# Kernel tuning notes

Hardware: AMD Instinct MI355X
Metric: run time of the kernel (lower is better)

Reference implementation:

```python
import jax, jax.numpy as jnp
import numpy as np

D_HIDDEN = 512
N_HEADS = 8
D_HEAD = D_HIDDEN // N_HEADS
LAYER_IDX = 0
FACTOR = 0.5 / float(np.sqrt(D_HEAD))


def setup_inputs() -> dict:
    key = jax.random.key(0)
    ks = jax.random.split(key, 16)
    B, N, d = 4, 2048, D_HIDDEN
    s = 1.0 / float(np.sqrt(d))
    inp = {
        "H": jax.random.normal(ks[0], (B, N, d), jnp.float32),
        "V": jax.random.normal(ks[1], (B, N, 3, d), jnp.float32),
        "D": jax.random.normal(ks[2], (B, N, N), jnp.float32),
        "rbf": jax.random.normal(ks[3], (1, B, 1, N, N), jnp.float32),
        "mask": jnp.ones((B, N), jnp.int32),
        # learned parameters (torch nn.Linear: y = x @ W.T + b)
        "Wq": jax.random.normal(ks[4], (4 * d, d), jnp.float32) * s,
        "bq": jax.random.normal(ks[5], (4 * d,), jnp.float32) * s,
        "Wk": jax.random.normal(ks[6], (4 * d, d), jnp.float32) * s,
        "bk": jax.random.normal(ks[7], (4 * d,), jnp.float32) * s,
        "Wv": jax.random.normal(ks[8], (d, d), jnp.float32) * s,
        "bv": jax.random.normal(ks[9], (d,), jnp.float32) * s,
        "Wvv": jax.random.normal(ks[10], (d, d), jnp.float32) * s,
        "Wo": jax.random.normal(ks[11], (d, d), jnp.float32) * s,
        "bo": jax.random.normal(ks[12], (d,), jnp.float32) * s,
        "Wvo": jax.random.normal(ks[13], (d, d), jnp.float32) * s,
    }
    return inp


def reference(H, V, D, rbf, mask, Wq, bq, Wk, bk, Wv, bv, Wvv, Wo, bo, Wvo):
    B, N, d = H.shape
    nh, dh = N_HEADS, D_HEAD
    # projections
    Hq = (H @ Wq.T + bq).reshape(B, N, nh, 4 * dh)
    Hk = (H @ Wk.T + bk).reshape(B, N, nh, 4 * dh)
    Hv = (H @ Wv.T + bv).reshape(B, N, nh, dh)
    # vector values: [B,N,3,nh,dh] -> [B,N,nh,3,dh] -> [B,N,nh,3*dh]
    Vv = (V @ Wvv.T).reshape(B, N, 3, nh, dh)
    Vv = jnp.swapaxes(Vv, -2, -3).reshape(B, N, nh, 3 * dh)
    V_attn = jnp.concatenate([Hv, Vv], axis=-1)  # [B,N,nh,4*dh]
    # additive geometric bias + key mask
    bias = rbf[LAYER_IDX] + D[:, None]  # [B,1,N,N]
    bias = jnp.where(mask[:, None, None, :] == 0, -jnp.inf, bias)
    # attention
    scores = jnp.einsum('bnhd,bmhd->bhnm', Hq, Hk) * FACTOR + bias
    attn = jax.nn.softmax(scores, axis=-1)
    res = jnp.einsum('bhnm,bmhd->bnhd', attn, V_attn)  # [B,N,nh,4*dh]
    # split scalar / vector outputs
    H_res = res[..., :dh].reshape(B, N, d)
    V_res = res[..., dh:].reshape(B, N, nh, 3, dh)
    V_res = jnp.swapaxes(V_res, -2, -3).reshape(B, N, 3, d)
    H_o = H_res @ Wo.T + bo
    V_o = V_res @ Wvo.T
    return H_o, V_o
```

## Files before the change

kernel.cpp:

```cpp
#include <hip/hip_runtime.h>
#include <hip/hip_bf16.h>
#include <stdint.h>

typedef __hip_bfloat16 bf16;
typedef __attribute__((ext_vector_type(8))) short bf16x8;
typedef __attribute__((ext_vector_type(4))) float f32x4;
typedef __attribute__((ext_vector_type(16))) float f32x16;
typedef __attribute__((ext_vector_type(4))) unsigned short u16x4;

#define DEVI __device__ __forceinline__

static constexpr float LOG2E = 1.44269504088896f;
static constexpr float FACTOR_L2E = 0.0625f * 1.44269504088896f;

DEVI unsigned short bfbits(float x) {
  return __builtin_bit_cast(unsigned short, __float2bfloat16(x));
}
DEVI float b2f(unsigned short u) {
  return __builtin_bit_cast(float, (uint32_t)u << 16);
}

__global__ void cvt_plain(const float* __restrict__ src, bf16* __restrict__ dst, int n) {
  int i = (blockIdx.x * 256 + threadIdx.x) * 4;
  if (i >= n) return;
  float4 v = *reinterpret_cast<const float4*>(src + i);
  union { unsigned short u[4]; uint64_t d; } t;
  t.u[0] = bfbits(v.x); t.u[1] = bfbits(v.y); t.u[2] = bfbits(v.z); t.u[3] = bfbits(v.w);
  *reinterpret_cast<uint64_t*>(dst + i) = t.d;
}

__global__ void cvt_vperm(const float* __restrict__ src, bf16* __restrict__ dst) {
  int g = blockIdx.x * 256 + threadIdx.x;
  int k4  = (g & 127) * 4;
  int rem = g >> 7;
  int c  = rem % 3;
  int bn = rem / 3;
  float4 v = *reinterpret_cast<const float4*>(src + (size_t)rem * 512 + k4);
  union { unsigned short u[4]; uint64_t d; } t;
  t.u[0] = bfbits(v.x); t.u[1] = bfbits(v.y); t.u[2] = bfbits(v.z); t.u[3] = bfbits(v.w);
  *reinterpret_cast<uint64_t*>(dst + ((size_t)c * 8192 + bn) * 512 + k4) = t.d;
}

__global__ void cvt_weights(const float* __restrict__ wq, const float* __restrict__ wk,
                            const float* __restrict__ wv, const float* __restrict__ wvv,
                            const float* __restrict__ wo, const float* __restrict__ wvo,
                            bf16* __restrict__ dst) {
  int blk = blockIdx.x;
  const float* s; int off;
  if      (blk < 1024) { s = wq  + blk * 1024;          off = 0       + blk * 1024; }
  else if (blk < 2048) { s = wk  + (blk - 1024) * 1024; off = 1048576 + (blk - 1024) * 1024; }
  else if (blk < 2304) { s = wv  + (blk - 2048) * 1024; off = 2097152 + (blk - 2048) * 1024; }
  else if (blk < 2560) { s = wvv + (blk - 2304) * 1024; off = 2359296 + (blk - 2304) * 1024; }
  else if (blk < 2816) { s = wo  + (blk - 2560) * 1024; off = 2621440 + (blk - 2560) * 1024; }
  else                 { s = wvo + (blk - 2816) * 1024; off = 2883584 + (blk - 2816) * 1024; }
  int i = threadIdx.x * 4;
  float4 v = *reinterpret_cast<const float4*>(s + i);
  union { unsigned short u[4]; uint64_t d; } t;
  t.u[0] = bfbits(v.x); t.u[1] = bfbits(v.y); t.u[2] = bfbits(v.z); t.u[3] = bfbits(v.w);
  *reinterpret_cast<uint64_t*>(dst + off + i) = t.d;
}

__global__ void bias_combine(const float* __restrict__ D, const float* __restrict__ rbf,
                             const int* __restrict__ mask, bf16* __restrict__ Bc) {
  size_t i = ((size_t)blockIdx.x * 256 + threadIdx.x) * 4;
  int col = (int)(i & 2047);
  int b   = (int)(i >> 22);
  float4 d = *reinterpret_cast<const float4*>(D + i);
  float4 r = *reinterpret_cast<const float4*>(rbf + i);
  const int* mrow = mask + b * 2048 + col;
  union { unsigned short u[4]; uint64_t dd; } t;
  t.u[0] = mrow[0] ? bfbits((d.x + r.x) * LOG2E) : bfbits(-1e30f);
  t.u[1] = mrow[1] ? bfbits((d.y + r.y) * LOG2E) : bfbits(-1e30f);
  t.u[2] = mrow[2] ? bfbits((d.z + r.z) * LOG2E) : bfbits(-1e30f);
  t.u[3] = mrow[3] ? bfbits((d.w + r.w) * LOG2E) : bfbits(-1e30f);
  *reinterpret_cast<uint64_t*>(Bc + i) = t.dd;
}

template<int MODE>
__global__ __launch_bounds__(256, 2) void gemm2(const bf16* __restrict__ A,
                                                const bf16* __restrict__ W,
                                                const bf16* __restrict__ W2,
                                                const float* __restrict__ bias,
                                                const float* __restrict__ bias2,
                                                void* __restrict__ outp) {
  constexpr int K = 512;
  __shared__ bf16 As[2][4096];
  __shared__ bf16 Bs[2][4096];
  const int tid = threadIdx.x;
  const int wid = tid >> 6, lane = tid & 63;
  const int lr = lane & 15, lg = lane >> 4;
  const int wr = wid >> 1, wc = wid & 1;
  const int bm = blockIdx.y * 128, bn = blockIdx.x * 128;

  const bf16* Wp;
  if constexpr (MODE == 0) Wp = W;
  else Wp = (blockIdx.y < 64) ? W : W2;

  const int q  = tid >> 2;
  const int ch = ((tid & 3) ^ ((tid >> 3) & 3)) * 8;
  const bf16* Asrc0 = A  + (size_t)(bm + q) * K + ch;
  const bf16* Asrc1 = A  + (size_t)(bm + 64 + q) * K + ch;
  const bf16* Wsrc0 = Wp + (size_t)(bn + q) * K + ch;
  const bf16* Wsrc1 = Wp + (size_t)(bn + 64 + q) * K + ch;
  const int wofs = wid * 1024;

  f32x4 acc[4][4];
#pragma unroll
  for (int m = 0; m < 4; m++)
#pragma unroll
    for (int n = 0; n < 4; n++) acc[m][n] = (f32x4){0.f, 0.f, 0.f, 0.f};

  __builtin_amdgcn_global_load_lds((const char*)Asrc0, (char*)&As[0][0] + wofs,        16, 0, 0);
  __builtin_amdgcn_global_load_lds((const char*)Asrc1, (char*)&As[0][0] + 4096 + wofs, 16, 0, 0);
  __builtin_amdgcn_global_load_lds((const char*)Wsrc0, (char*)&Bs[0][0] + wofs,        16, 0, 0);
  __builtin_amdgcn_global_load_lds((const char*)Wsrc1, (char*)&Bs[0][0] + 4096 + wofs, 16, 0, 0);
  __syncthreads();

  const int fxor = ((lr >> 1) & 3) << 4;
  for (int kt = 0; kt < 16; ++kt) {
    const int cur = kt & 1;
    if (kt < 15) {
      const int nxt = cur ^ 1;
      __builtin_amdgcn_global_load_lds((const char*)(Asrc0 + (kt + 1) * 32), (char*)&As[nxt][0] + wofs,        16, 0, 0);
      __builtin_amdgcn_global_load_lds((const char*)(Asrc1 + (kt + 1) * 32), (char*)&As[nxt][0] + 4096 + wofs, 16, 0, 0);
      __builtin_amdgcn_global_load_lds((const char*)(Wsrc0 + (kt + 1) * 32), (char*)&Bs[nxt][0] + wofs,        16, 0, 0);
      __builtin_amdgcn_global_load_lds((const char*)(Wsrc1 + (kt + 1) * 32), (char*)&Bs[nxt][0] + 4096 + wofs, 16, 0, 0);
    }
    const char* AsC = (const char*)&As[cur][0];
    const char* BsC = (const char*)&Bs[cur][0];
    bf16x8 af[4], bfr[4];
#pragma unroll
    for (int m = 0; m < 4; m++) {
      const int row = wr * 64 + m * 16 + lr;
      af[m] = *reinterpret_cast<const bf16x8*>(AsC + row * 64 + ((lg << 4) ^ fxor));
    }
#pragma unroll
    for (int n = 0; n < 4; n++) {
      const int row = wc * 64 + n * 16 + lr;
      bfr[n] = *reinterpret_cast<const bf16x8*>(BsC + row * 64 + ((lg << 4) ^ fxor));
    }
#pragma unroll
    for (int m = 0; m < 4; m++)
#pragma unroll
      for (int n = 0; n < 4; n++)
        acc[m][n] = __builtin_amdgcn_mfma_f32_16x16x32_bf16(af[m], bfr[n], acc[m][n], 0, 0, 0);
    __syncthreads();
  }

#pragma unroll
  for (int m = 0; m < 4; m++) {
#pragma unroll
    for (int n = 0; n < 4; n++) {
      const int col  = bn + wc * 64 + n * 16 + lr;
      const int row0 = bm + wr * 64 + m * 16 + lg * 4;
      if constexpr (MODE == 0) {
        const int isK = col >> 11;
        const int col2 = col & 2047;
        const float bb = isK ? bias2[col2] : bias[col2];
        const int hh = col2 >> 8, t = col2 & 255;
        bf16* out = (bf16*)outp + (size_t)isK * 16777216;
#pragma unroll
        for (int qq = 0; qq < 4; qq++) {
          const int row = row0 + qq;
          const int b = row >> 11, nn = row & 2047;
          float v = acc[m][n][qq] + bb;
          if (!isK) v *= FACTOR_L2E;
          out[(size_t)((b * 8 + hh) * 2048 + nn) * 256 + t] = __float2bfloat16(v);
        }
      } else if constexpr (MODE == 1) {
        bf16* out = (bf16*)outp;
        const int hh = col >> 6, t = col & 63;
        int dimrow, nn; float bb;
        if (row0 < 8192) {
          const int b = row0 >> 11; nn = row0 & 2047;
          dimrow = (b * 8 + hh) * 256 + t;
          bb = bias[col];
        } else {
          const int r = row0 - 8192;
          const int c = r >> 13, b = (r >> 11) & 3; nn = r & 2047;
          dimrow = (b * 8 + hh) * 256 + 64 + c * 64 + t;
          bb = 0.f;
        }
        const int i4 = (nn >> 2) & 7;
        const int o4 = (i4 & 4) | ((i4 & 1) << 1) | ((i4 >> 1) & 1);
        const int nn2 = (nn & ~31) | (o4 << 2);
        union { unsigned short u[4]; uint64_t d; } pk;
#pragma unroll
        for (int qq = 0; qq < 4; qq++) pk.u[qq] = bfbits(acc[m][n][qq] + bb);
        *reinterpret_cast<uint64_t*>(out + (size_t)dimrow * 2048 + nn2) = pk.d;
      } else {
        float* out = (float*)outp;
        if (row0 < 8192) {
          const float bb = bias[col];
#pragma unroll
          for (int qq = 0; qq < 4; qq++)
            out[(size_t)(row0 + qq) * 512 + col] = acc[m][n][qq] + bb;
        } else {
#pragma unroll
          for (int qq = 0; qq < 4; qq++)
            out[4194304 + (size_t)(row0 - 8192 + qq) * 512 + col] = acc[m][n][qq];
        }
      }
    }
  }
}

__global__ __launch_bounds__(512, 1) void attn_kernel(
    const bf16* __restrict__ Qg, const bf16* __restrict__ Kg, const bf16* __restrict__ Vtg,
    const bf16* __restrict__ Bc, bf16* __restrict__ Hres, bf16* __restrict__ Vres) {
  __shared__ bf16 Ks[4][32 * 256];
  __shared__ bf16 Vs[4][256 * 32];

  const int g = blockIdx.x;
  const int x = g & 7, loc = g >> 3;
  const int bh = x * 4 + (loc & 3);
  const int qt = loc >> 2;
  const int b = bh >> 3, h = bh & 7;
  const int tid = threadIdx.x, w = tid >> 6, lane = tid & 63;
  const int lq = lane & 31, hi = lane >> 5;
  const int q0 = qt * 256 + w * 32;

  const bf16* Qb = Qg + (size_t)bh * 2048 * 256;
  const char* KbC = (const char*)(Kg + (size_t)bh * 2048 * 256);
  const char* VbC = (const char*)(Vtg + (size_t)bh * 256 * 2048);
  const bf16* Bb = Bc + ((size_t)(b * 2048 + q0 + lq)) * 2048 + hi * 4;

  bf16x8 qf[16];
#pragma unroll
  for (int kc = 0; kc < 16; kc++)
    qf[kc] = *reinterpret_cast<const bf16x8*>(Qb + (size_t)(q0 + lq) * 256 + kc * 16 + hi * 8);

  f32x16 O[8];
#pragma unroll
  for (int dt = 0; dt < 8; dt++)
#pragma unroll
    for (int r = 0; r < 16; r++) O[dt][r] = 0.f;
  float mrun = -INFINITY, lrun = 0.f;

  const char* ksrc[2]; const char* vsrc[2];
#pragma unroll
  for (int i = 0; i < 2; i++) {
    const int X = w * 2048 + i * 1024 + lane * 16;
    const int krow = X >> 9, kcol = X & 511;
    ksrc[i] = KbC + (size_t)krow * 512 + (kcol ^ ((krow & 31) << 4));
    const int vrow = X >> 6;
    const int gg = ((vrow >> 1) ^ (vrow >> 3)) & 3;
    vsrc[i] = VbC + (size_t)vrow * 4096 + (((lane & 3) ^ gg) << 4);
  }
  char* ldsK = (char*)Ks + w * 2048;
  char* ldsV = (char*)Vs + w * 2048;

  u16x4 bg[8];
#pragma unroll
  for (int i = 0; i < 4; i++) {
    bg[i]     = *reinterpret_cast<const u16x4*>(Bb + i * 8);
    bg[4 + i] = *reinterpret_cast<const u16x4*>(Bb + 32 + i * 8);
  }
  __builtin_amdgcn_sched_barrier(0);
#pragma unroll
  for (int hh = 0; hh < 2; hh++) {
#pragma unroll
    for (int i = 0; i < 2; i++) {
      __builtin_amdgcn_global_load_lds(ksrc[i] + (size_t)hh * 16384, ldsK + hh * 16384 + i * 1024, 16, 0, 0);
      __builtin_amdgcn_global_load_lds(vsrc[i] + (size_t)hh * 64,    ldsV + hh * 16384 + i * 1024, 16, 0, 0);
    }
  }
  __builtin_amdgcn_sched_barrier(0);
  asm volatile("s_waitcnt vmcnt(0)" ::: "memory");
  __builtin_amdgcn_sched_barrier(0);
  __builtin_amdgcn_s_barrier();

#pragma unroll 1
  for (int kt = 0; kt < 32; ++kt) {
    const int buf = kt & 1;
    const int nb = (buf ^ 1) * 2;
    const int tn = (kt < 31) ? 2 * kt + 2 : 62;

#pragma unroll
    for (int hh = 0; hh < 2; hh++) {
#pragma unroll
      for (int i = 0; i < 2; i++) {
        __builtin_amdgcn_global_load_lds(ksrc[i] + (size_t)(tn + hh) * 16384, ldsK + (nb + hh) * 16384 + i * 1024, 16, 0, 0);
        __builtin_amdgcn_global_load_lds(vsrc[i] + (size_t)(tn + hh) * 64,    ldsV + (nb + hh) * 16384 + i * 1024, 16, 0, 0);
      }
    }
    __builtin_amdgcn_sched_barrier(0);

    {
      const char* KsC = (const char*)Ks + (buf * 2 + 0) * 16384;
      const char* VsC = (const char*)Vs + (buf * 2 + 0) * 16384;
      f32x16 s;
#pragma unroll
      for (int r = 0; r < 16; r++) s[r] = 0.f;
      const int kxor = lq << 4;
#pragma unroll
      for (int kc = 0; kc < 16; kc++) {
        bf16x8 kf = *reinterpret_cast<const bf16x8*>(KsC + lq * 512 + ((kc * 32 + hi * 16) ^ kxor));
        s = __builtin_amdgcn_mfma_f32_32x32x16_bf16(kf, qf[kc], s, 0, 0, 0);
      }
#pragma unroll
      for (int r = 0; r < 16; r++)
        s[r] += b2f((unsigned short)bg[r >> 2][r & 3]);

      float m0 = fmaxf(s[0], s[1]),  m1 = fmaxf(s[2], s[3]);
      float m2 = fmaxf(s[4], s[5]),  m3 = fmaxf(s[6], s[7]);
      float m4 = fmaxf(s[8], s[9]),  m5 = fmaxf(s[10], s[11]);
      float m6 = fmaxf(s[12], s[13]), m7 = fmaxf(s[14], s[15]);
      float pmax = fmaxf(fmaxf(fmaxf(m0, m1), fmaxf(m2, m3)),
                         fmaxf(fmaxf(m4, m5), fmaxf(m6, m7)));
      pmax = fmaxf(pmax, __shfl_xor(pmax, 32));

      const bool ok = (pmax <= mrun + 8.f);
      if (!__all((int)ok)) {
        const float mnew = fmaxf(mrun, pmax);
        const float scq = exp2f(mrun - mnew);
        mrun = mnew;
        lrun *= scq;
        float sfac[16];
#pragma unroll
        for (int r = 0; r < 16; r++) sfac[r] = __shfl(scq, (r & 3) + 8 * (r >> 2) + 4 * hi);
#pragma unroll
        for (int dt = 0; dt < 8; dt++)
#pragma unroll
          for (int r = 0; r < 16; r++) O[dt][r] *= sfac[r];
      }

      union { unsigned short u[8]; bf16x8 v; } pa0, pa1;
      float rs = 0.f;
#pragma unroll
      for (int j = 0; j < 8; j++) {
        const float p = exp2f(s[j] - mrun);
        pa0.u[j] = bfbits(p);
        rs += b2f(pa0.u[j]);
      }
#pragma unroll
      for (int j = 0; j < 8; j++) {
        const float p = exp2f(s[8 + j] - mrun);
        pa1.u[j] = bfbits(p);
        rs += b2f(pa1.u[j]);
      }
      rs += __shfl_xor(rs, 32);
      lrun += rs;

#pragma unroll
      for (int dt = 0; dt < 8; dt++) {
        const int row = dt * 32 + lq;
        const int gg = ((row >> 1) ^ (row >> 3)) & 3;
        bf16x8 v0 = *reinterpret_cast<const bf16x8*>(VsC + row * 64 + ((hi ^ gg) << 4));
        bf16x8 v1 = *reinterpret_cast<const bf16x8*>(VsC + row * 64 + (((2 + hi) ^ gg) << 4));
        O[dt] = __builtin_amdgcn_mfma_f32_32x32x16_bf16(pa0.v, v0, O[dt], 0, 0, 0);
        O[dt] = __builtin_amdgcn_mfma_f32_32x32x16_bf16(pa1.v, v1, O[dt], 0, 0, 0);
      }
    }

    {
      const char* KsC = (const char*)Ks + (buf * 2 + 1) * 16384;
      const char* VsC = (const char*)Vs + (buf * 2 + 1) * 16384;
      f32x16 s;
#pragma unroll
      for (int r = 0; r < 16; r++) s[r] = 0.f;
      const int kxor = lq << 4;
#pragma unroll
      for (int kc = 0; kc < 16; kc++) {
        bf16x8 kf = *reinterpret_cast<const bf16x8*>(KsC + lq * 512 + ((kc * 32 + hi * 16) ^ kxor));
        s = __builtin_amdgcn_mfma_f32_32x32x16_bf16(kf, qf[kc], s, 0, 0, 0);
      }
#pragma unroll
      for (int r = 0; r < 16; r++)
        s[r] += b2f((unsigned short)bg[4 + (r >> 2)][r & 3]);

#pragma unroll
      for (int i = 0; i < 4; i++) {
        bg[i]     = *reinterpret_cast<const u16x4*>(Bb + (size_t)tn * 32 + i * 8);
        bg[4 + i] = *reinterpret_cast<const u16x4*>(Bb + (size_t)(tn + 1) * 32 + i * 8);
      }

      float m0 = fmaxf(s[0], s[1]),  m1 = fmaxf(s[2], s[3]);
      float m2 = fmaxf(s[4], s[5]),  m3 = fmaxf(s[6], s[7]);
      float m4 = fmaxf(s[8], s[9]),  m5 = fmaxf(s[10], s[11]);
      float m6 = fmaxf(s[12], s[13]), m7 = fmaxf(s[14], s[15]);
      float pmax = fmaxf(fmaxf(fmaxf(m0, m1), fmaxf(m2, m3)),
                         fmaxf(fmaxf(m4, m5), fmaxf(m6, m7)));
      pmax = fmaxf(pmax, __shfl_xor(pmax, 32));

      const bool ok = (pmax <= mrun + 8.f);
      if (!__all((int)ok)) {
        const float mnew = fmaxf(mrun, pmax);
        const float scq = exp2f(mrun - mnew);
        mrun = mnew;
        lrun *= scq;
        float sfac[16];
#pragma unroll
        for (int r = 0; r < 16; r++) sfac[r] = __shfl(scq, (r & 3) + 8 * (r >> 2) + 4 * hi);
#pragma unroll
        for (int dt = 0; dt < 8; dt++)
#pragma unroll
          for (int r = 0; r < 16; r++) O[dt][r] *= sfac[r];
      }

      union { unsigned short u[8]; bf16x8 v; } pa0, pa1;
      float rs = 0.f;
#pragma unroll
      for (int j = 0; j < 8; j++) {
        const float p = exp2f(s[j] - mrun);
        pa0.u[j] = bfbits(p);
        rs += b2f(pa0.u[j]);
      }
#pragma unroll
      for (int j = 0; j < 8; j++) {
        const float p = exp2f(s[8 + j] - mrun);
        pa1.u[j] = bfbits(p);
        rs += b2f(pa1.u[j]);
      }
      rs += __shfl_xor(rs, 32);
      lrun += rs;

#pragma unroll
      for (int dt = 0; dt < 8; dt++) {
        const int row = dt * 32 + lq;
        const int gg = ((row >> 1) ^ (row >> 3)) & 3;
        bf16x8 v0 = *reinterpret_cast<const bf16x8*>(VsC + row * 64 + ((hi ^ gg) << 4));
        bf16x8 v1 = *reinterpret_cast<const bf16x8*>(VsC + row * 64 + (((2 + hi) ^ gg) << 4));
        O[dt] = __builtin_amdgcn_mfma_f32_32x32x16_bf16(pa0.v, v0, O[dt], 0, 0, 0);
        O[dt] = __builtin_amdgcn_mfma_f32_32x32x16_bf16(pa1.v, v1, O[dt], 0, 0, 0);
      }
    }

    asm volatile("s_waitcnt vmcnt(0)" ::: "memory");
    __builtin_amdgcn_sched_barrier(0);
    __builtin_amdgcn_s_barrier();
  }

  const float rli = 1.0f / lrun;
  float rl[16];
#pragma unroll
  for (int r = 0; r < 16; r++) rl[r] = __shfl(rli, (r & 3) + 8 * (r >> 2) + 4 * hi);
#pragma unroll
  for (int dt = 0; dt < 8; dt++) {
    const int d = dt * 32 + lq;
#pragma unroll
    for (int r = 0; r < 16; r++) {
      const int row = q0 + (r & 3) + 8 * (r >> 2) + 4 * hi;
      const float v = O[dt][r] * rl[r];
      if (d < 64) {
        Hres[(size_t)(b * 2048 + row) * 512 + h * 64 + d] = __float2bfloat16(v);
      } else {
        const int c = (d - 64) >> 6, t = (d - 64) & 63;
        Vres[((size_t)(b * 2048 + row) * 3 + c) * 512 + h * 64 + t] = __float2bfloat16(v);
      }
    }
  }
}

extern "C" void kernel_launch(void* const* d_in, const int* in_sizes, int n_in,
                              void* d_out, int out_size, void* d_ws, size_t ws_size,
                              hipStream_t stream) {
  const float* H   = (const float*)d_in[0];
  const float* V   = (const float*)d_in[1];
  const float* Dm  = (const float*)d_in[2];
  const float* rbf = (const float*)d_in[3];
  const int*   mask= (const int*)d_in[4];
  const float* Wq  = (const float*)d_in[5];
  const float* bq  = (const float*)d_in[6];
  const float* Wk  = (const float*)d_in[7];
  const float* bk  = (const float*)d_in[8];
  const float* Wv  = (const float*)d_in[9];
  const float* bv  = (const float*)d_in[10];
  const float* Wvv = (const float*)d_in[11];
  const float* Wo  = (const float*)d_in[12];
  const float* bo  = (const float*)d_in[13];
  const float* Wvo = (const float*)d_in[14];

  char* ws = (char*)d_ws;
  bf16* Hbf  = (bf16*)(ws);
  bf16* Wall = (bf16*)(ws + 33554432);
  bf16* Qw   = (bf16*)(ws + 39845888);
  bf16* Kw   = Qw + 16777216;
  bf16* Vtw  = (bf16*)(ws + 106954752);
  bf16* Hres = Hbf;
  bf16* Wqb  = Wall;
  bf16* Wvb  = Wall + 2097152;
  bf16* Wvvb = Wall + 2359296;
  bf16* Wob  = Wall + 2621440;
  bf16* Wvob = Wall + 2883584;
  bf16* Bcb  = (bf16*)d_out;

  bias_combine<<<16384, 256, 0, stream>>>(Dm, rbf, mask, Bcb);
  cvt_plain<<<4096, 256, 0, stream>>>(H, Hbf, 4194304);
  cvt_vperm<<<12288, 256, 0, stream>>>(V, Hbf + 4194304);
  cvt_weights<<<3072, 256, 0, stream>>>(Wq, Wk, Wv, Wvv, Wo, Wvo, Wall);

  gemm2<0><<<dim3(32, 64), 256, 0, stream>>>(Hbf, Wqb, nullptr, bq, bk, Qw);
  gemm2<1><<<dim3(4, 256), 256, 0, stream>>>(Hbf, Wvb, Wvvb, bv, nullptr, Vtw);

  attn_kernel<<<256, 512, 0, stream>>>(Qw, Kw, Vtw, Bcb, Hres, Hbf + 4194304);

  gemm2<2><<<dim3(4, 256), 256, 0, stream>>>(Hbf, Wob, Wvob, bo, nullptr, d_out);
}
```

Before: 485.0 us.

## Software-pipeline QK^T one tile ahead with a 4-slot ring buffer

The attention loop is rewritten so that the QK^T MFMA for tile t+1 is issued before the softmax and PV MFMAs of tile t. This lets the tensor-core work overlap the exp and reduction work. The two-tile double buffer, which waited on vmcnt(0), becomes a four-slot rotating ring. Loads are prefetched two tiles ahead and only the older group is waited on with vmcnt(4). The bias load is also moved one iteration earlier. In exchange, register pressure rises from the extra live score accumulator, and there are twice as many barriers per key.

```diff
diff --git a/kernel.cpp b/kernel.cpp
--- a/kernel.cpp
+++ b/kernel.cpp
@@ -250,185 +250,190 @@
   char* ldsK = (char*)Ks + w * 2048;
   char* ldsV = (char*)Vs + w * 2048;
 
-  u16x4 bg[8];
-#pragma unroll
-  for (int i = 0; i < 4; i++) {
-    bg[i]     = *reinterpret_cast<const u16x4*>(Bb + i * 8);
-    bg[4 + i] = *reinterpret_cast<const u16x4*>(Bb + 32 + i * 8);
+  const int kxor = lq << 4;
+
+#pragma unroll
+  for (int i = 0; i < 2; i++) {
+    __builtin_amdgcn_global_load_lds(ksrc[i], ldsK + i * 1024, 16, 0, 0);
+    __builtin_amdgcn_global_load_lds(vsrc[i], ldsV + i * 1024, 16, 0, 0);
   }
   __builtin_amdgcn_sched_barrier(0);
 #pragma unroll
-  for (int hh = 0; hh < 2; hh++) {
-#pragma unroll
-    for (int i = 0; i < 2; i++) {
-      __builtin_amdgcn_global_load_lds(ksrc[i] + (size_t)hh * 16384, ldsK + hh * 16384 + i * 1024, 16, 0, 0);
-      __builtin_amdgcn_global_load_lds(vsrc[i] + (size_t)hh * 64,    ldsV + hh * 16384 + i * 1024, 16, 0, 0);
-    }
+  for (int i = 0; i < 2; i++) {
+    __builtin_amdgcn_global_load_lds(ksrc[i] + 16384, ldsK + 16384 + i * 1024, 16, 0, 0);
+    __builtin_amdgcn_global_load_lds(vsrc[i] + 64,    ldsV + 16384 + i * 1024, 16, 0, 0);
   }
   __builtin_amdgcn_sched_barrier(0);
-  asm volatile("s_waitcnt vmcnt(0)" ::: "memory");
+  asm volatile("s_waitcnt vmcnt(4)" ::: "memory");
   __builtin_amdgcn_sched_barrier(0);
   __builtin_amdgcn_s_barrier();
 
+  f32x16 s_cur;
+#pragma unroll
+  for (int r = 0; r < 16; r++) s_cur[r] = 0.f;
+#pragma unroll
+  for (int kc = 0; kc < 16; kc++) {
+    bf16x8 kf = *reinterpret_cast<const bf16x8*>((const char*)Ks + lq * 512 + ((kc * 32 + hi * 16) ^ kxor));
+    s_cur = __builtin_amdgcn_mfma_f32_32x32x16_bf16(kf, qf[kc], s_cur, 0, 0, 0);
+  }
+  u16x4 bgA[4];
+#pragma unroll
+  for (int i = 0; i < 4; i++) bgA[i] = *reinterpret_cast<const u16x4*>(Bb + i * 8);
+  __builtin_amdgcn_sched_barrier(0);
+#pragma unroll
+  for (int i = 0; i < 2; i++) {
+    __builtin_amdgcn_global_load_lds(ksrc[i] + 2 * 16384, ldsK + 2 * 16384 + i * 1024, 16, 0, 0);
+    __builtin_amdgcn_global_load_lds(vsrc[i] + 2 * 64,    ldsV + 2 * 16384 + i * 1024, 16, 0, 0);
+  }
+  __builtin_amdgcn_sched_barrier(0);
+  asm volatile("s_waitcnt vmcnt(4)" ::: "memory");
+  __builtin_amdgcn_sched_barrier(0);
+  __builtin_amdgcn_s_barrier();
+
+  int cq = 1, cp = 0, cs = 3;
+
 #pragma unroll 1
-  for (int kt = 0; kt < 32; ++kt) {
-    const int buf = kt & 1;
-    const int nb = (buf ^ 1) * 2;
-    const int tn = (kt < 31) ? 2 * kt + 2 : 62;
-
-#pragma unroll
-    for (int hh = 0; hh < 2; hh++) {
+  for (int t = 1; t < 64; ++t) {
+    u16x4 bgB[4];
+#pragma unroll
+    for (int i = 0; i < 4; i++)
+      bgB[i] = *reinterpret_cast<const u16x4*>(Bb + (size_t)t * 32 + i * 8);
+    __builtin_amdgcn_sched_barrier(0);
+    {
+      const int tn = (t < 62) ? t + 2 : 63;
 #pragma unroll
       for (int i = 0; i < 2; i++) {
-        __builtin_amdgcn_global_load_lds(ksrc[i] + (size_t)(tn + hh) * 16384, ldsK + (nb + hh) * 16384 + i * 1024, 16, 0, 0);
-        __builtin_amdgcn_global_load_lds(vsrc[i] + (size_t)(tn + hh) * 64,    ldsV + (nb + hh) * 16384 + i * 1024, 16, 0, 0);
+        __builtin_amdgcn_global_load_lds(ksrc[i] + (size_t)tn * 16384, ldsK + cs * 16384 + i * 1024, 16, 0, 0);
+        __builtin_amdgcn_global_load_lds(vsrc[i] + (size_t)tn * 64,    ldsV + cs * 16384 + i * 1024, 16, 0, 0);
       }
     }
     __builtin_amdgcn_sched_barrier(0);
 
-    {
-      const char* KsC = (const char*)Ks + (buf * 2 + 0) * 16384;
-      const char* VsC = (const char*)Vs + (buf * 2 + 0) * 16384;
-      f32x16 s;
-#pragma unroll
-      for (int r = 0; r < 16; r++) s[r] = 0.f;
-      const int kxor = lq << 4;
-#pragma unroll
-      for (int kc = 0; kc < 16; kc++) {
-        bf16x8 kf = *reinterpret_cast<const bf16x8*>(KsC + lq * 512 + ((kc * 32 + hi * 16) ^ kxor));
-        s = __builtin_amdgcn_mfma_f32_32x32x16_bf16(kf, qf[kc], s, 0, 0, 0);
-      }
-#pragma unroll
-      for (int r = 0; r < 16; r++)
-        s[r] += b2f((unsigned short)bg[r >> 2][r & 3]);
-
-      float m0 = fmaxf(s[0], s[1]),  m1 = fmaxf(s[2], s[3]);
-      float m2 = fmaxf(s[4], s[5]),  m3 = fmaxf(s[6], s[7]);
-      float m4 = fmaxf(s[8], s[9]),  m5 = fmaxf(s[10], s[11]);
-      float m6 = fmaxf(s[12], s[13]), m7 = fmaxf(s[14], s[15]);
-      float pmax = fmaxf(fmaxf(fmaxf(m0, m1), fmaxf(m2, m3)),
-                         fmaxf(fmaxf(m4, m5), fmaxf(m6, m7)));
-      pmax = fmaxf(pmax, __shfl_xor(pmax, 32));
-
-      const bool ok = (pmax <= mrun + 8.f);
-      if (!__all((int)ok)) {
-        const float mnew = fmaxf(mrun, pmax);
-        const float scq = exp2f(mrun - mnew);
-        mrun = mnew;
-        lrun *= scq;
-        float sfac[16];
-#pragma unroll
-        for (int r = 0; r < 16; r++) sfac[r] = __shfl(scq, (r & 3) + 8 * (r >> 2) + 4 * hi);
-#pragma unroll
-        for (int dt = 0; dt < 8; dt++)
-#pragma unroll
-          for (int r = 0; r < 16; r++) O[dt][r] *= sfac[r];
-      }
-
-      union { unsigned short u[8]; bf16x8 v; } pa0, pa1;
-      float rs = 0.f;
-#pragma unroll
-      for (int j = 0; j < 8; j++) {
-        const float p = exp2f(s[j] - mrun);
-        pa0.u[j] = bfbits(p);
-        rs += b2f(pa0.u[j]);
-      }
-#pragma unroll
-      for (int j = 0; j < 8; j++) {
-        const float p = exp2f(s[8 + j] - mrun);
-        pa1.u[j] = bfbits(p);
-        rs += b2f(pa1.u[j]);
-      }
-      rs += __shfl_xor(rs, 32);
-      lrun += rs;
-
-#pragma unroll
-      for (int dt = 0; dt < 8; dt++) {
-        const int row = dt * 32 + lq;
-        const int gg = ((row >> 1) ^ (row >> 3)) & 3;
-        bf16x8 v0 = *reinterpret_cast<const bf16x8*>(VsC + row * 64 + ((hi ^ gg) << 4));
-        bf16x8 v1 = *reinterpret_cast<const bf16x8*>(VsC + row * 64 + (((2 + hi) ^ gg) << 4));
-        O[dt] = __builtin_amdgcn_mfma_f32_32x32x16_bf16(pa0.v, v0, O[dt], 0, 0, 0);
-        O[dt] = __builtin_amdgcn_mfma_f32_32x32x16_bf16(pa1.v, v1, O[dt], 0, 0, 0);
-      }
-    }
-
-    {
-      const char* KsC = (const char*)Ks + (buf * 2 + 1) * 16384;
-      const char* VsC = (const char*)Vs + (buf * 2 + 1) * 16384;
-      f32x16 s;
-#pragma unroll
-      for (int r = 0; r < 16; r++) s[r] = 0.f;
-      const int kxor = lq << 4;
-#pragma unroll
-      for (int kc = 0; kc < 16; kc++) {
-        bf16x8 kf = *reinterpret_cast<const bf16x8*>(KsC + lq * 512 + ((kc * 32 + hi * 16) ^ kxor));
-        s = __builtin_amdgcn_mfma_f32_32x32x16_bf16(kf, qf[kc], s, 0, 0, 0);
-      }
-#pragma unroll
-      for (int r = 0; r < 16; r++)
-        s[r] += b2f((unsigned short)bg[4 + (r >> 2)][r & 3]);
-
-#pragma unroll
-      for (int i = 0; i < 4; i++) {
-        bg[i]     = *reinterpret_cast<const u16x4*>(Bb + (size_t)tn * 32 + i * 8);
-        bg[4 + i] = *reinterpret_cast<const u16x4*>(Bb + (size_t)(tn + 1) * 32 + i * 8);
-      }
-
-      float m0 = fmaxf(s[0], s[1]),  m1 = fmaxf(s[2], s[3]);
-      float m2 = fmaxf(s[4], s[5]),  m3 = fmaxf(s[6], s[7]);
-      float m4 = fmaxf(s[8], s[9]),  m5 = fmaxf(s[10], s[11]);
-      float m6 = fmaxf(s[12], s[13]), m7 = fmaxf(s[14], s[15]);
-      float pmax = fmaxf(fmaxf(fmaxf(m0, m1), fmaxf(m2, m3)),
-                         fmaxf(fmaxf(m4, m5), fmaxf(m6, m7)));
-      pmax = fmaxf(pmax, __shfl_xor(pmax, 32));
-
-      const bool ok = (pmax <= mrun + 8.f);
-      if (!__all((int)ok)) {
-        const float mnew = fmaxf(mrun, pmax);
-        const float scq = exp2f(mrun - mnew);
-        mrun = mnew;
-        lrun *= scq;
-        float sfac[16];
-#pragma unroll
-        for (int r = 0; r < 16; r++) sfac[r] = __shfl(scq, (r & 3) + 8 * (r >> 2) + 4 * hi);
-#pragma unroll
-        for (int dt = 0; dt < 8; dt++)
-#pragma unroll
-          for (int r = 0; r < 16; r++) O[dt][r] *= sfac[r];
-      }
-
-      union { unsigned short u[8]; bf16x8 v; } pa0, pa1;
-      float rs = 0.f;
-#pragma unroll
-      for (int j = 0; j < 8; j++) {
-        const float p = exp2f(s[j] - mrun);
-        pa0.u[j] = bfbits(p);
-        rs += b2f(pa0.u[j]);
-      }
-#pragma unroll
-      for (int j = 0; j < 8; j++) {
-        const float p = exp2f(s[8 + j] - mrun);
-        pa1.u[j] = bfbits(p);
-        rs += b2f(pa1.u[j]);
-      }
-      rs += __shfl_xor(rs, 32);
-      lrun += rs;
-
-#pragma unroll
-      for (int dt = 0; dt < 8; dt++) {
-        const int row = dt * 32 + lq;
-        const int gg = ((row >> 1) ^ (row >> 3)) & 3;
-        bf16x8 v0 = *reinterpret_cast<const bf16x8*>(VsC + row * 64 + ((hi ^ gg) << 4));
-        bf16x8 v1 = *reinterpret_cast<const bf16x8*>(VsC + row * 64 + (((2 + hi) ^ gg) << 4));
-        O[dt] = __builtin_amdgcn_mfma_f32_32x32x16_bf16(pa0.v, v0, O[dt], 0, 0, 0);
-        O[dt] = __builtin_amdgcn_mfma_f32_32x32x16_bf16(pa1.v, v1, O[dt], 0, 0, 0);
-      }
-    }
-
-    asm volatile("s_waitcnt vmcnt(0)" ::: "memory");
+    f32x16 sn;
+#pragma unroll
+    for (int r = 0; r < 16; r++) sn[r] = 0.f;
+    const char* KsC = (const char*)Ks + cq * 16384;
+#pragma unroll
+    for (int kc = 0; kc < 16; kc++) {
+      bf16x8 kf = *reinterpret_cast<const bf16x8*>(KsC + lq * 512 + ((kc * 32 + hi * 16) ^ kxor));
+      sn = __builtin_amdgcn_mfma_f32_32x32x16_bf16(kf, qf[kc], sn, 0, 0, 0);
+    }
+
+    float sc[16];
+#pragma unroll
+    for (int r = 0; r < 16; r++)
+      sc[r] = s_cur[r] + b2f((unsigned short)bgA[r >> 2][r & 3]);
+    float m0 = fmaxf(sc[0], sc[1]),  m1 = fmaxf(sc[2], sc[3]);
+    float m2 = fmaxf(sc[4], sc[5]),  m3 = fmaxf(sc[6], sc[7]);
+    float m4 = fmaxf(sc[8], sc[9]),  m5 = fmaxf(sc[10], sc[11]);
+    float m6 = fmaxf(sc[12], sc[13]), m7 = fmaxf(sc[14], sc[15]);
+    float pmax = fmaxf(fmaxf(fmaxf(m0, m1), fmaxf(m2, m3)),
+                       fmaxf(fmaxf(m4, m5), fmaxf(m6, m7)));
+    pmax = fmaxf(pmax, __shfl_xor(pmax, 32));
+    const bool ok = (pmax <= mrun + 8.f);
+    if (!__all((int)ok)) {
+      const float mnew = fmaxf(mrun, pmax);
+      const float scq = exp2f(mrun - mnew);
+      mrun = mnew;
+      lrun *= scq;
+      float sfac[16];
+#pragma unroll
+      for (int r = 0; r < 16; r++) sfac[r] = __shfl(scq, (r & 3) + 8 * (r >> 2) + 4 * hi);
+#pragma unroll
+      for (int dt = 0; dt < 8; dt++)
+#pragma unroll
+        for (int r = 0; r < 16; r++) O[dt][r] *= sfac[r];
+    }
+    union { unsigned short u[8]; bf16x8 v; } pa0, pa1;
+    float rs = 0.f;
+#pragma unroll
+    for (int j = 0; j < 8; j++) {
+      const float p = exp2f(sc[j] - mrun);
+      pa0.u[j] = bfbits(p);
+      rs += b2f(pa0.u[j]);
+    }
+#pragma unroll
+    for (int j = 0; j < 8; j++) {
+      const float p = exp2f(sc[8 + j] - mrun);
+      pa1.u[j] = bfbits(p);
+      rs += b2f(pa1.u[j]);
+    }
+    rs += __shfl_xor(rs, 32);
+    lrun += rs;
+
+    const char* VsC = (const char*)Vs + cp * 16384;
+#pragma unroll
+    for (int dt = 0; dt < 8; dt++) {
+      const int row = dt * 32 + lq;
+      const int gg = ((row >> 1) ^ (row >> 3)) & 3;
+      bf16x8 v0 = *reinterpret_cast<const bf16x8*>(VsC + row * 64 + ((hi ^ gg) << 4));
+      bf16x8 v1 = *reinterpret_cast<const bf16x8*>(VsC + row * 64 + (((2 + hi) ^ gg) << 4));
+      O[dt] = __builtin_amdgcn_mfma_f32_32x32x16_bf16(pa0.v, v0, O[dt], 0, 0, 0);
+      O[dt] = __builtin_amdgcn_mfma_f32_32x32x16_bf16(pa1.v, v1, O[dt], 0, 0, 0);
+    }
+
+    asm volatile("s_waitcnt vmcnt(4)" ::: "memory");
     __builtin_amdgcn_sched_barrier(0);
     __builtin_amdgcn_s_barrier();
+
+    s_cur = sn;
+#pragma unroll
+    for (int i = 0; i < 4; i++) bgA[i] = bgB[i];
+    cq = (cq + 1) & 3; cp = (cp + 1) & 3; cs = (cs + 1) & 3;
+  }
+
+  {
+    float sc[16];
+#pragma unroll
+    for (int r = 0; r < 16; r++)
+      sc[r] = s_cur[r] + b2f((unsigned short)bgA[r >> 2][r & 3]);
+    float m0 = fmaxf(sc[0], sc[1]),  m1 = fmaxf(sc[2], sc[3]);
+    float m2 = fmaxf(sc[4], sc[5]),  m3 = fmaxf(sc[6], sc[7]);
+    float m4 = fmaxf(sc[8], sc[9]),  m5 = fmaxf(sc[10], sc[11]);
+    float m6 = fmaxf(sc[12], sc[13]), m7 = fmaxf(sc[14], sc[15]);
+    float pmax = fmaxf(fmaxf(fmaxf(m0, m1), fmaxf(m2, m3)),
+                       fmaxf(fmaxf(m4, m5), fmaxf(m6, m7)));
+    pmax = fmaxf(pmax, __shfl_xor(pmax, 32));
+    const bool ok = (pmax <= mrun + 8.f);
+    if (!__all((int)ok)) {
+      const float mnew = fmaxf(mrun, pmax);
+      const float scq = exp2f(mrun - mnew);
+      mrun = mnew;
+      lrun *= scq;
+      float sfac[16];
+#pragma unroll
+      for (int r = 0; r < 16; r++) sfac[r] = __shfl(scq, (r & 3) + 8 * (r >> 2) + 4 * hi);
+#pragma unroll
+      for (int dt = 0; dt < 8; dt++)
+#pragma unroll
+        for (int r = 0; r < 16; r++) O[dt][r] *= sfac[r];
+    }
+    union { unsigned short u[8]; bf16x8 v; } pa0, pa1;
+    float rs = 0.f;
+#pragma unroll
+    for (int j = 0; j < 8; j++) {
+      const float p = exp2f(sc[j] - mrun);
+      pa0.u[j] = bfbits(p);
+      rs += b2f(pa0.u[j]);
+    }
+#pragma unroll
+    for (int j = 0; j < 8; j++) {
+      const float p = exp2f(sc[8 + j] - mrun);
+      pa1.u[j] = bfbits(p);
+      rs += b2f(pa1.u[j]);
+    }
+    rs += __shfl_xor(rs, 32);
+    lrun += rs;
+    const char* VsC = (const char*)Vs + cp * 16384;
+#pragma unroll
+    for (int dt = 0; dt < 8; dt++) {
+      const int row = dt * 32 + lq;
+      const int gg = ((row >> 1) ^ (row >> 3)) & 3;
+      bf16x8 v0 = *reinterpret_cast<const bf16x8*>(VsC + row * 64 + ((hi ^ gg) << 4));
+      bf16x8 v1 = *reinterpret_cast<const bf16x8*>(VsC + row * 64 + (((2 + hi) ^ gg) << 4));
+      O[dt] = __builtin_amdgcn_mfma_f32_32x32x16_bf16(pa0.v, v0, O[dt], 0, 0, 0);
+      O[dt] = __builtin_amdgcn_mfma_f32_32x32x16_bf16(pa1.v, v1, O[dt], 0, 0, 0);
+    }
   }
 
   const float rli = 1.0f / lrun;
```

Result: slower. 512.2 us (+5.6%).
